# Performance work log

Hardware: AMD Instinct MI355X
Metric: run time of the kernel (lower is better)

## Reference

```python
import jax, jax.numpy as jnp
import numpy as np

THR = 0.2
TEMPERATURE = 0.1


def setup_inputs() -> dict:
    key = jax.random.key(0)
    k0, k1 = jax.random.split(key)
    N, L, S, C = 4, 4096, 4096, 256
    feat_c0 = jax.random.normal(k0, (N, L, C), dtype=jnp.float32)
    feat_c1 = jax.random.normal(k1, (N, S, C), dtype=jnp.float32)
    return {"feat_c0": feat_c0, "feat_c1": feat_c1}


def reference(feat_c0, feat_c1):
    C = feat_c0.shape[-1]
    scale = 1.0 / (float(C) ** 0.5)
    f0 = feat_c0 * scale  # [N, L, C]
    f1 = feat_c1 * scale  # [N, S, C]

    # sim_matrix = -cdist(f0, f1) / temperature / C  (Euclidean distance)
    sq0 = jnp.sum(f0 * f0, axis=-1)  # [N, L]
    sq1 = jnp.sum(f1 * f1, axis=-1)  # [N, S]
    inner = jnp.einsum('nlc,nsc->nls', f0, f1)  # [N, L, S]
    d2 = jnp.maximum(sq0[:, :, None] + sq1[:, None, :] - 2.0 * inner, 0.0)
    dist = jnp.sqrt(d2)
    sim_matrix = -dist / (TEMPERATURE * C)

    # dual softmax
    conf_matrix0 = jax.nn.softmax(sim_matrix, axis=1)
    conf_matrix1 = jax.nn.softmax(sim_matrix, axis=2)
    conf_matrix = conf_matrix0 * conf_matrix1

    # mutual-nearest-neighbor + threshold matching (dense, jit-friendly form)
    mask = conf_matrix > THR
    i_mask = conf_matrix == jnp.max(conf_matrix, axis=2, keepdims=True)
    j_mask = conf_matrix == jnp.max(conf_matrix, axis=1, keepdims=True)
    mask = mask & i_mask & j_mask  # [N, L, S]

    mask_v = jnp.any(mask, axis=2)                  # [N, L] — row i has a match
    all_j_ids = jnp.argmax(mask, axis=2)            # [N, L] — matched column j
    mconf = jnp.take_along_axis(conf_matrix, all_j_ids[:, :, None], axis=2)[:, :, 0]
    mconf = jnp.where(mask_v, mconf, 0.0)           # [N, L] dense match confidence

    return (conf_matrix, conf_matrix0, conf_matrix1, sim_matrix,
            mask_v, all_j_ids, mconf)
```

## Files before the change

kernel.cpp:

```cpp
#include <hip/hip_runtime.h>
#include <stdint.h>

#define NB 4
#define LD 4096
#define SD 4096
#define CD 256

static constexpr long CHUNK = (long)NB * LD * SD;
static constexpr float SCALE = 0.0625f;
static constexpr float INV_TC = 1.0f / 25.6f;
static constexpr float THRV = 0.2f;

typedef __attribute__((ext_vector_type(8))) short bf16x8;
typedef __attribute__((ext_vector_type(4))) float f32x4;

__device__ __forceinline__ unsigned short f2bf(float x) {
  unsigned int u = __float_as_uint(x);
  return (unsigned short)((u + 0x7FFFu + ((u >> 16) & 1u)) >> 16);
}

__device__ __forceinline__ void gload_lds16(const void* g, void* l) {
  __builtin_amdgcn_global_load_lds((const __attribute__((address_space(1))) void*)g,
                                   (__attribute__((address_space(3))) void*)l, 16, 0, 0);
}

__device__ __forceinline__ void nt_store4(f32x4 v, float* p) {
  __builtin_nontemporal_store(v, (f32x4*)p);
}

__global__ __launch_bounds__(256) void k_prep(const float* __restrict__ f0,
                                              const float* __restrict__ f1,
                                              unsigned short* __restrict__ abf,
                                              unsigned short* __restrict__ bbf,
                                              float* __restrict__ sq0,
                                              float* __restrict__ sq1) {
  int wid = threadIdx.x >> 6, lane = threadIdx.x & 63;
  long row = (long)blockIdx.x * 4 + wid;
  const long nl = (long)NB * LD;
  const float* src;
  unsigned short* dst;
  float* sqd;
  if (row < nl) {
    src = f0 + row * CD; dst = abf + row * CD; sqd = sq0 + row;
  } else {
    long r = row - nl;
    src = f1 + r * CD; dst = bbf + r * CD; sqd = sq1 + r;
  }
  f32x4 v = *reinterpret_cast<const f32x4*>(src + lane * 4);
  v *= SCALE;
  ushort4 o;
  o.x = f2bf(v[0]); o.y = f2bf(v[1]); o.z = f2bf(v[2]); o.w = f2bf(v[3]);
  reinterpret_cast<ushort4*>(dst)[lane] = o;
  float s = v[0] * v[0] + v[1] * v[1] + v[2] * v[2] + v[3] * v[3];
  #pragma unroll
  for (int m = 1; m < 64; m <<= 1) s += __shfl_xor(s, m);
  if (lane == 0) *sqd = s;
}

__device__ __forceinline__ void gemm_core(const char* aB, const char* bB, char* lds,
                                          int t, f32x4 (&acc)[4][4]) {
  int wid = t >> 6, lane = t & 63;
  int srow = t >> 3;
  int scolb = (t & 7) << 4;
  int wrb = (wid >> 1) << 6;
  int wcb = (wid & 1) << 6;
  int lrow = lane & 15;
  int kgrp = lane >> 4;

  #pragma unroll
  for (int m = 0; m < 4; ++m)
    #pragma unroll
    for (int n = 0; n < 4; ++n)
      acc[m][n] = (f32x4){0.f, 0.f, 0.f, 0.f};

  for (int kt = 0; kt < 4; ++kt) {
    #pragma unroll
    for (int i = 0; i < 4; ++i) {
      int row = i * 32 + srow;
      int sc = scolb ^ ((row & 7) << 4);
      gload_lds16(aB + (long)row * (CD * 2) + kt * 128 + sc,
                  lds + i * 4096 + (wid << 10));
      gload_lds16(bB + (long)row * (CD * 2) + kt * 128 + sc,
                  lds + 16384 + i * 4096 + (wid << 10));
    }
    __syncthreads();
    #pragma unroll
    for (int ks = 0; ks < 2; ++ks) {
      int kb = ks * 64 + kgrp * 16;
      bf16x8 af[4], bfr[4];
      #pragma unroll
      for (int m = 0; m < 4; ++m) {
        int r = wrb + m * 16 + lrow;
        af[m] = *(const bf16x8*)(lds + r * 128 + (kb ^ ((r & 7) << 4)));
      }
      #pragma unroll
      for (int n = 0; n < 4; ++n) {
        int r = wcb + n * 16 + lrow;
        bfr[n] = *(const bf16x8*)(lds + 16384 + r * 128 + (kb ^ ((r & 7) << 4)));
      }
      #pragma unroll
      for (int m = 0; m < 4; ++m)
        #pragma unroll
        for (int n = 0; n < 4; ++n)
          acc[m][n] = __builtin_amdgcn_mfma_f32_16x16x32_bf16(af[m], bfr[n], acc[m][n], 0, 0, 0);
    }
    __syncthreads();
  }
}

__global__ __launch_bounds__(256) void k_gemm(const unsigned short* __restrict__ abf,
                                              const unsigned short* __restrict__ bbf,
                                              const float* __restrict__ sq0,
                                              const float* __restrict__ sq1,
                                              float* __restrict__ simout,
                                              float* __restrict__ rowsum,
                                              float* __restrict__ colsum) {
  __shared__ char lds[33792];
  int t = threadIdx.x;
  int wid = t >> 6, lane = t & 63;
  int wrb = (wid >> 1) << 6, wcb = (wid & 1) << 6;
  int lrow = lane & 15, kgrp = lane >> 4;

  int wg = blockIdx.x;
  int swz = (wg & 7) * 512 + (wg >> 3);
  int bz = swz >> 10;
  int rem = swz & 1023;
  long tileM = (long)(rem >> 5) * 128;
  long tileS = (long)(rem & 31) * 128;
  const char* aB = (const char*)(abf + ((long)bz * LD + tileM) * CD);
  const char* bB = (const char*)(bbf + ((long)bz * SD + tileS) * CD);

  f32x4 acc[4][4];
  gemm_core(aB, bB, lds, t, acc);

  long gcol0 = (long)bz * SD + tileS + wcb;
  float sq1v[4];
  #pragma unroll
  for (int n = 0; n < 4; ++n) sq1v[n] = sq1[gcol0 + n * 16 + lrow];

  float ce[4] = {0.f, 0.f, 0.f, 0.f};
  float* ltile = (float*)lds;

  #pragma unroll
  for (int h = 0; h < 2; ++h) {
    __syncthreads();
    #pragma unroll
    for (int mm = 0; mm < 2; ++mm) {
      int m = 2 * h + mm;
      #pragma unroll
      for (int i = 0; i < 4; ++i) {
        int lr = m * 16 + kgrp * 4 + i;
        long gl = tileM + wrb + lr;
        float s0 = sq0[(long)bz * LD + gl];
        int q = (wid >> 1) * 32 + mm * 16 + kgrp * 4 + i;
        float rs = 0.f;
        #pragma unroll
        for (int n = 0; n < 4; ++n) {
          float inner = acc[m][n][i];
          float d2 = fmaxf(s0 + sq1v[n] - 2.0f * inner, 0.f);
          float sv = -__builtin_sqrtf(d2) * INV_TC;
          ltile[q * 132 + wcb + n * 16 + lrow] = sv;
          float e = __expf(sv);
          rs += e;
          ce[n] += e;
        }
        #pragma unroll
        for (int d = 1; d < 16; d <<= 1) rs += __shfl_xor(rs, d);
        if (lrow == 0) atomicAdd(&rowsum[(long)bz * LD + gl], rs);
      }
    }
    __syncthreads();
    #pragma unroll
    for (int j = 0; j < 8; ++j) {
      int f = t + 256 * j;
      int r = f >> 5;
      int c4 = f & 31;
      long grow = tileM + (r >> 5) * 64 + 32 * h + (r & 31);
      f32x4 v = *(const f32x4*)&ltile[r * 132 + c4 * 4];
      *(f32x4*)(simout + ((long)bz * LD + grow) * SD + tileS + c4 * 4) = v;
    }
  }

  #pragma unroll
  for (int n = 0; n < 4; ++n) {
    float cs = ce[n];
    cs += __shfl_xor(cs, 16);
    cs += __shfl_xor(cs, 32);
    if (kgrp == 0) atomicAdd(&colsum[gcol0 + n * 16 + lrow], cs);
  }
}

__global__ __launch_bounds__(256) void k_softmax(const float* __restrict__ sim,
                                                 const float* __restrict__ rowsum,
                                                 const float* __restrict__ colsum,
                                                 float* __restrict__ conf,
                                                 float* __restrict__ conf0,
                                                 float* __restrict__ conf1,
                                                 unsigned long long* __restrict__ rowpack,
                                                 unsigned long long* __restrict__ colpack) {
  __shared__ unsigned long long rmx[64];
  __shared__ unsigned long long cmx[512];
  int t = threadIdx.x;
  int w = t >> 6, lane = t & 63;
  cmx[t] = 0ull;
  cmx[t + 256] = 0ull;
  __syncthreads();

  int n = blockIdx.z;
  long rbase = (long)blockIdx.y * 64;
  long cbase = (long)blockIdx.x * 512;

  float invc[2][4];
  unsigned long long cpk[2][4];
  #pragma unroll
  for (int it = 0; it < 2; ++it) {
    f32x4 cs = *(const f32x4*)(colsum + (long)n * SD + cbase + it * 256 + lane * 4);
    invc[it][0] = 1.0f / cs[0]; invc[it][1] = 1.0f / cs[1];
    invc[it][2] = 1.0f / cs[2]; invc[it][3] = 1.0f / cs[3];
    cpk[it][0] = cpk[it][1] = cpk[it][2] = cpk[it][3] = 0ull;
  }

  #pragma unroll 2
  for (int j = 0; j < 16; ++j) {
    int r = w + j * 4;
    long gr = rbase + r;
    float invr = 1.0f / rowsum[(long)n * LD + gr];
    long rowoff = ((long)n * LD + gr) * SD + cbase;
    unsigned long long rbest = 0ull;
    #pragma unroll
    for (int it = 0; it < 2; ++it) {
      long idx = rowoff + it * 256 + lane * 4;
      f32x4 sv = *(const f32x4*)(sim + idx);
      f32x4 cf, c0v, c1v;
      #pragma unroll
      for (int q = 0; q < 4; ++q) {
        float e = __expf(sv[q]);
        float a0 = e * invc[it][q];
        float a1 = e * invr;
        float c = a0 * a1;
        c0v[q] = a0;
        c1v[q] = a1;
        cf[q] = c;
        unsigned long long pk = ((unsigned long long)__float_as_uint(c) << 32) |
                                (unsigned int)(~(unsigned int)(cbase + it * 256 + lane * 4 + q));
        rbest = pk > rbest ? pk : rbest;
        cpk[it][q] = pk > cpk[it][q] ? pk : cpk[it][q];
      }
      nt_store4(cf, conf + idx);
      nt_store4(c0v, conf0 + idx);
      nt_store4(c1v, conf1 + idx);
    }
    #pragma unroll
    for (int d = 1; d < 64; d <<= 1) {
      unsigned long long o = __shfl_xor(rbest, d);
      rbest = o > rbest ? o : rbest;
    }
    if (lane == 0) rmx[r] = rbest;
  }
  #pragma unroll
  for (int it = 0; it < 2; ++it)
    #pragma unroll
    for (int q = 0; q < 4; ++q)
      atomicMax(&cmx[it * 256 + lane * 4 + q], cpk[it][q]);
  __syncthreads();
  if (t < 64) atomicMax(&rowpack[(long)n * LD + rbase + t], rmx[t]);
  atomicMax(&colpack[(long)n * SD + cbase + t], cmx[t]);
  atomicMax(&colpack[(long)n * SD + cbase + 256 + t], cmx[t + 256]);
}

__global__ __launch_bounds__(256) void k_final(const unsigned long long* __restrict__ rowpack,
                                               const unsigned long long* __restrict__ colpack,
                                               float* __restrict__ maskv,
                                               float* __restrict__ jids,
                                               float* __restrict__ mconf) {
  long idx = (long)blockIdx.x * 256 + threadIdx.x;
  if (idx >= (long)NB * LD) return;
  int n = (int)(idx / LD);
  unsigned long long rp = rowpack[idx];
  unsigned int cbits = (unsigned int)(rp >> 32);
  float cval = __uint_as_float(cbits);
  unsigned int col = ~(unsigned int)rp;
  bool valid = (cval > THRV) && (col < (unsigned int)SD);
  if (valid) {
    unsigned long long cp = colpack[(long)n * SD + col];
    valid = ((unsigned int)(cp >> 32)) == cbits;
  }
  maskv[idx] = valid ? 1.0f : 0.0f;
  jids[idx]  = valid ? (float)col : 0.0f;
  mconf[idx] = valid ? cval : 0.0f;
}

extern "C" void kernel_launch(void* const* d_in, const int* in_sizes, int n_in,
                              void* d_out, int out_size, void* d_ws, size_t ws_size,
                              hipStream_t stream) {
  const float* f0 = (const float*)d_in[0];
  const float* f1 = (const float*)d_in[1];
  float* out = (float*)d_out;
  float* conf  = out;
  float* conf0 = out + CHUNK;
  float* conf1 = out + 2 * CHUNK;
  float* simo  = out + 3 * CHUNK;
  float* maskv = out + 4 * CHUNK;
  float* jids  = maskv + (long)NB * LD;
  float* mconf = jids + (long)NB * LD;

  char* ws = (char*)d_ws;
  unsigned short* abf = (unsigned short*)ws;
  unsigned short* bbf = (unsigned short*)(ws + 8388608);
  float* sq0 = (float*)(ws + 16777216);
  float* sq1 = (float*)(ws + 16777216 + 65536);
  char* accums = ws + 16908288;
  float* rowsum = (float*)accums;
  float* colsum = (float*)(accums + 65536);
  unsigned long long* rowpack = (unsigned long long*)(accums + 131072);
  unsigned long long* colpack = (unsigned long long*)(accums + 262144);
  (void)hipMemsetAsync(accums, 0, 393216, stream);

  k_prep<<<dim3((NB * (LD + SD)) / 4), dim3(256), 0, stream>>>(f0, f1, abf, bbf, sq0, sq1);
  k_gemm<<<dim3(4096), dim3(256), 0, stream>>>(abf, bbf, sq0, sq1, simo, rowsum, colsum);
  k_softmax<<<dim3(SD / 512, LD / 64, NB), dim3(256), 0, stream>>>(simo, rowsum, colsum,
                                                                   conf, conf0, conf1,
                                                                   rowpack, colpack);
  k_final<<<dim3((NB * LD + 255) / 256), dim3(256), 0, stream>>>(rowpack, colpack,
                                                                 maskv, jids, mconf);
}
```

Measured before the change: 368.5 us.

## Load GEMM fragments directly from global memory, bypassing LDS staging

Drops the LDS-staged K loop (global_load_lds plus two barriers per K tile) in the similarity GEMM. Each wave now loads its bf16 A/B MFMA fragments straight from global memory into registers and fully unrolls the 8 K-steps. Launch bounds gain an occupancy hint of 3 blocks per CU. This removes the barriers and LDS traffic, but each fragment row is now fetched by both waves that share it, and the loads are strided and less coalesced, so more L2/global traffic is traded for less synchronisation. The larger unrolled register footprint may also conflict with the occupancy target.

```diff
diff --git a/kernel.cpp b/kernel.cpp
--- a/kernel.cpp
+++ b/kernel.cpp
@@ -17,11 +17,6 @@
 __device__ __forceinline__ unsigned short f2bf(float x) {
   unsigned int u = __float_as_uint(x);
   return (unsigned short)((u + 0x7FFFu + ((u >> 16) & 1u)) >> 16);
-}
-
-__device__ __forceinline__ void gload_lds16(const void* g, void* l) {
-  __builtin_amdgcn_global_load_lds((const __attribute__((address_space(1))) void*)g,
-                                   (__attribute__((address_space(3))) void*)l, 16, 0, 0);
 }
 
 __device__ __forceinline__ void nt_store4(f32x4 v, float* p) {
@@ -57,64 +52,13 @@
   if (lane == 0) *sqd = s;
 }
 
-__device__ __forceinline__ void gemm_core(const char* aB, const char* bB, char* lds,
-                                          int t, f32x4 (&acc)[4][4]) {
-  int wid = t >> 6, lane = t & 63;
-  int srow = t >> 3;
-  int scolb = (t & 7) << 4;
-  int wrb = (wid >> 1) << 6;
-  int wcb = (wid & 1) << 6;
-  int lrow = lane & 15;
-  int kgrp = lane >> 4;
-
-  #pragma unroll
-  for (int m = 0; m < 4; ++m)
-    #pragma unroll
-    for (int n = 0; n < 4; ++n)
-      acc[m][n] = (f32x4){0.f, 0.f, 0.f, 0.f};
-
-  for (int kt = 0; kt < 4; ++kt) {
-    #pragma unroll
-    for (int i = 0; i < 4; ++i) {
-      int row = i * 32 + srow;
-      int sc = scolb ^ ((row & 7) << 4);
-      gload_lds16(aB + (long)row * (CD * 2) + kt * 128 + sc,
-                  lds + i * 4096 + (wid << 10));
-      gload_lds16(bB + (long)row * (CD * 2) + kt * 128 + sc,
-                  lds + 16384 + i * 4096 + (wid << 10));
-    }
-    __syncthreads();
-    #pragma unroll
-    for (int ks = 0; ks < 2; ++ks) {
-      int kb = ks * 64 + kgrp * 16;
-      bf16x8 af[4], bfr[4];
-      #pragma unroll
-      for (int m = 0; m < 4; ++m) {
-        int r = wrb + m * 16 + lrow;
-        af[m] = *(const bf16x8*)(lds + r * 128 + (kb ^ ((r & 7) << 4)));
-      }
-      #pragma unroll
-      for (int n = 0; n < 4; ++n) {
-        int r = wcb + n * 16 + lrow;
-        bfr[n] = *(const bf16x8*)(lds + 16384 + r * 128 + (kb ^ ((r & 7) << 4)));
-      }
-      #pragma unroll
-      for (int m = 0; m < 4; ++m)
-        #pragma unroll
-        for (int n = 0; n < 4; ++n)
-          acc[m][n] = __builtin_amdgcn_mfma_f32_16x16x32_bf16(af[m], bfr[n], acc[m][n], 0, 0, 0);
-    }
-    __syncthreads();
-  }
-}
-
-__global__ __launch_bounds__(256) void k_gemm(const unsigned short* __restrict__ abf,
-                                              const unsigned short* __restrict__ bbf,
-                                              const float* __restrict__ sq0,
-                                              const float* __restrict__ sq1,
-                                              float* __restrict__ simout,
-                                              float* __restrict__ rowsum,
-                                              float* __restrict__ colsum) {
+__global__ __launch_bounds__(256, 3) void k_gemm(const unsigned short* __restrict__ abf,
+                                                 const unsigned short* __restrict__ bbf,
+                                                 const float* __restrict__ sq0,
+                                                 const float* __restrict__ sq1,
+                                                 float* __restrict__ simout,
+                                                 float* __restrict__ rowsum,
+                                                 float* __restrict__ colsum) {
   __shared__ char lds[33792];
   int t = threadIdx.x;
   int wid = t >> 6, lane = t & 63;
@@ -127,11 +71,32 @@
   int rem = swz & 1023;
   long tileM = (long)(rem >> 5) * 128;
   long tileS = (long)(rem & 31) * 128;
-  const char* aB = (const char*)(abf + ((long)bz * LD + tileM) * CD);
-  const char* bB = (const char*)(bbf + ((long)bz * SD + tileS) * CD);
+
+  const unsigned short* aP = abf + ((long)bz * LD + tileM + wrb + lrow) * CD + kgrp * 8;
+  const unsigned short* bP = bbf + ((long)bz * SD + tileS + wcb + lrow) * CD + kgrp * 8;
 
   f32x4 acc[4][4];
-  gemm_core(aB, bB, lds, t, acc);
+  #pragma unroll
+  for (int m = 0; m < 4; ++m)
+    #pragma unroll
+    for (int n = 0; n < 4; ++n)
+      acc[m][n] = (f32x4){0.f, 0.f, 0.f, 0.f};
+
+  #pragma unroll
+  for (int s8 = 0; s8 < 8; ++s8) {
+    bf16x8 af[4], bfr[4];
+    #pragma unroll
+    for (int m = 0; m < 4; ++m)
+      af[m] = *(const bf16x8*)(aP + m * 16 * CD + s8 * 32);
+    #pragma unroll
+    for (int n = 0; n < 4; ++n)
+      bfr[n] = *(const bf16x8*)(bP + n * 16 * CD + s8 * 32);
+    #pragma unroll
+    for (int m = 0; m < 4; ++m)
+      #pragma unroll
+      for (int n = 0; n < 4; ++n)
+        acc[m][n] = __builtin_amdgcn_mfma_f32_16x16x32_bf16(af[m], bfr[n], acc[m][n], 0, 0, 0);
+  }
 
   long gcol0 = (long)bz * SD + tileS + wcb;
   float sq1v[4];
```

Measured after the change: 382.7 us. 3.9% more time.

## Double-buffer GEMM K-loop with padded k-major LDS layout and occupancy hint

Applied to the files above, without the earlier changes.

Restructures the GEMM main loop into eight 32-wide K steps that use two LDS buffers, so the global-to-LDS load for the next step is issued while MFMAs run on the current one. This also removes one barrier per iteration. The LDS layout changes from a row-major XOR-swizzled tile to k-group-major slabs padded to 2064 bytes, which avoids bank conflicts without the swizzle arithmetic. It also adds a launch_bounds min-blocks hint of 4 to limit registers and raise occupancy. The risks are register spilling under the tighter bound and a smaller K step per barrier.

```diff
diff --git a/kernel.cpp b/kernel.cpp
--- a/kernel.cpp
+++ b/kernel.cpp
@@ -57,11 +57,23 @@
   if (lane == 0) *sqd = s;
 }
 
+__device__ __forceinline__ void stage32(const char* aB, const char* bB, char* lbuf,
+                                        int kt, int t) {
+  #pragma unroll
+  for (int i = 0; i < 2; ++i) {
+    int s = t + i * 256;
+    int ks = s >> 7;
+    int r = s & 127;
+    long goff = (long)r * (CD * 2) + kt * 64 + ks * 16;
+    int loff = ks * 2064 + r * 16;
+    gload_lds16(aB + goff, lbuf + loff);
+    gload_lds16(bB + goff, lbuf + 8256 + loff);
+  }
+}
+
 __device__ __forceinline__ void gemm_core(const char* aB, const char* bB, char* lds,
                                           int t, f32x4 (&acc)[4][4]) {
   int wid = t >> 6, lane = t & 63;
-  int srow = t >> 3;
-  int scolb = (t & 7) << 4;
   int wrb = (wid >> 1) << 6;
   int wcb = (wid & 1) << 6;
   int lrow = lane & 15;
@@ -73,48 +85,38 @@
     for (int n = 0; n < 4; ++n)
       acc[m][n] = (f32x4){0.f, 0.f, 0.f, 0.f};
 
-  for (int kt = 0; kt < 4; ++kt) {
-    #pragma unroll
-    for (int i = 0; i < 4; ++i) {
-      int row = i * 32 + srow;
-      int sc = scolb ^ ((row & 7) << 4);
-      gload_lds16(aB + (long)row * (CD * 2) + kt * 128 + sc,
-                  lds + i * 4096 + (wid << 10));
-      gload_lds16(bB + (long)row * (CD * 2) + kt * 128 + sc,
-                  lds + 16384 + i * 4096 + (wid << 10));
-    }
+  stage32(aB, bB, lds, 0, t);
+  __syncthreads();
+
+  #pragma unroll
+  for (int kt = 0; kt < 8; ++kt) {
+    char* cur = lds + (kt & 1) * 16512;
+    if (kt < 7)
+      stage32(aB, bB, lds + ((kt + 1) & 1) * 16512, kt + 1, t);
+    int kbp = kgrp * 2064;
+    bf16x8 af[4], bfr[4];
+    #pragma unroll
+    for (int m = 0; m < 4; ++m)
+      af[m] = *(const bf16x8*)(cur + kbp + (wrb + m * 16 + lrow) * 16);
+    #pragma unroll
+    for (int n = 0; n < 4; ++n)
+      bfr[n] = *(const bf16x8*)(cur + 8256 + kbp + (wcb + n * 16 + lrow) * 16);
+    #pragma unroll
+    for (int m = 0; m < 4; ++m)
+      #pragma unroll
+      for (int n = 0; n < 4; ++n)
+        acc[m][n] = __builtin_amdgcn_mfma_f32_16x16x32_bf16(af[m], bfr[n], acc[m][n], 0, 0, 0);
     __syncthreads();
-    #pragma unroll
-    for (int ks = 0; ks < 2; ++ks) {
-      int kb = ks * 64 + kgrp * 16;
-      bf16x8 af[4], bfr[4];
-      #pragma unroll
-      for (int m = 0; m < 4; ++m) {
-        int r = wrb + m * 16 + lrow;
-        af[m] = *(const bf16x8*)(lds + r * 128 + (kb ^ ((r & 7) << 4)));
-      }
-      #pragma unroll
-      for (int n = 0; n < 4; ++n) {
-        int r = wcb + n * 16 + lrow;
-        bfr[n] = *(const bf16x8*)(lds + 16384 + r * 128 + (kb ^ ((r & 7) << 4)));
-      }
-      #pragma unroll
-      for (int m = 0; m < 4; ++m)
-        #pragma unroll
-        for (int n = 0; n < 4; ++n)
-          acc[m][n] = __builtin_amdgcn_mfma_f32_16x16x32_bf16(af[m], bfr[n], acc[m][n], 0, 0, 0);
-    }
-    __syncthreads();
-  }
-}
-
-__global__ __launch_bounds__(256) void k_gemm(const unsigned short* __restrict__ abf,
-                                              const unsigned short* __restrict__ bbf,
-                                              const float* __restrict__ sq0,
-                                              const float* __restrict__ sq1,
-                                              float* __restrict__ simout,
-                                              float* __restrict__ rowsum,
-                                              float* __restrict__ colsum) {
+  }
+}
+
+__global__ __launch_bounds__(256, 4) void k_gemm(const unsigned short* __restrict__ abf,
+                                                 const unsigned short* __restrict__ bbf,
+                                                 const float* __restrict__ sq0,
+                                                 const float* __restrict__ sq1,
+                                                 float* __restrict__ simout,
+                                                 float* __restrict__ rowsum,
+                                                 float* __restrict__ colsum) {
   __shared__ char lds[33792];
   int t = threadIdx.x;
   int wid = t >> 6, lane = t & 63;
```

Result: faster. 346.3 us (-6.0%).
